# Performance work log

Hardware: AMD Instinct MI355X
Metric: run time of the kernel (lower is better)

## Reference

```python
import jax, jax.numpy as jnp
import numpy as np

N, L, D = 64, 1024, 512
SPAN = 8
LI = L - 2            # inner length after stripping CLS and last token
S = LI // SPAN        # 127 spans per sample
OUT = 300
EPS = 1e-5


def setup_inputs() -> dict:
    key = jax.random.key(0)
    k1, k2, k3 = jax.random.split(key, 3)
    t1 = jax.random.normal(k1, (N, L, D), dtype=jnp.float32)
    # contiguous non-empty spans (start, end) into the inner sequence, same for each sample
    starts = np.arange(S, dtype=np.int64) * SPAN
    ends = starts + SPAN
    word_seq = jnp.asarray(np.broadcast_to(np.stack([starts, ends], -1), (N, S, 2)).copy())
    key_padding_mask = jnp.zeros((N, S), dtype=bool)
    w_lin = jax.random.normal(k2, (OUT, D), dtype=jnp.float32) * (1.0 / np.sqrt(D))
    b_lin = jax.random.normal(k3, (OUT,), dtype=jnp.float32) * 0.02
    gamma = jnp.ones((OUT,), dtype=jnp.float32)
    beta = jnp.zeros((OUT,), dtype=jnp.float32)
    return {"t1": t1, "word_seq": word_seq, "key_padding_mask": key_padding_mask,
            "w_lin": w_lin, "b_lin": b_lin, "gamma": gamma, "beta": beta}


def reference(t1, word_seq, key_padding_mask, w_lin, b_lin, gamma, beta):
    use = t1[:, 0]                      # (N, D) cls token
    inner = t1[:, 1:-1, :]              # (N, LI, D)
    li = inner.shape[1]
    # prefix sums -> span sums via one gather (replaces per-span mean kernels)
    prefix = jnp.concatenate([jnp.zeros_like(inner[:, :1]), jnp.cumsum(inner, axis=1)], axis=1)  # (N, LI+1, D)
    start = jnp.minimum(word_seq[..., 0], li - 1)   # (N, S)
    end = jnp.minimum(word_seq[..., 1], li)
    span_sum = (jnp.take_along_axis(prefix, end[..., None], axis=1)
                - jnp.take_along_axis(prefix, start[..., None], axis=1))  # (N, S, D)
    count = (end - start).astype(inner.dtype)[..., None]                   # (N, S, 1) all > 0
    means = span_sum / count
    # linear_ then LayerNorm
    h = jnp.einsum('nsd,od->nso', means, w_lin) + b_lin                    # (N, S, OUT)
    mu = jnp.mean(h, axis=-1, keepdims=True)
    var = jnp.mean(jnp.square(h - mu), axis=-1, keepdims=True)
    out = (h - mu) * jax.lax.rsqrt(var + EPS) * gamma + beta
    return (out, use)
```

## Files before the change

kernel.cpp:

```cpp
#include <hip/hip_runtime.h>
#include <hip/hip_bf16.h>
#include <stdint.h>

#define N_   64
#define L_   1024
#define D_   512
#define S_   127
#define OUT_ 300
#define NT_  20
#define OUTP (NT_*16)
#define EPS_ 1e-5f
#define M_TOTAL (N_*S_)
#define BM 16
#define BK 64
#define NBLK (M_TOTAL/BM)
#define ASTR 72
#define BSTR 72
#define HSTR 320

typedef __attribute__((ext_vector_type(4))) float  float4v;
typedef __attribute__((ext_vector_type(8))) __bf16 bf16x8;
typedef __attribute__((ext_vector_type(4))) __bf16 bf16x4;

__global__ void conv_w_kernel(const float* __restrict__ w, __bf16* __restrict__ wbf) {
    int idx = blockIdx.x * 256 + threadIdx.x;
    int o = idx >> 9, d = idx & (D_ - 1);
    float v = (o < OUT_) ? w[o * D_ + d] : 0.0f;
    wbf[idx] = (__bf16)v;
}

__global__ void use_copy_kernel(const float* __restrict__ t1, float* __restrict__ ou) {
    int idx = blockIdx.x * 256 + threadIdx.x;
    int n = idx >> 7, dg = idx & 127;
    float4v v = *(const float4v*)(t1 + (size_t)n * L_ * D_ + dg * 4);
    *(float4v*)(ou + n * D_ + dg * 4) = v;
}

__global__ __launch_bounds__(256) void enc_main(
    const float* __restrict__ t1, const int* __restrict__ wseq,
    const __bf16* __restrict__ wbf, const float* __restrict__ b_lin,
    const float* __restrict__ gamma, const float* __restrict__ beta,
    float* __restrict__ out)
{
    __shared__ __align__(16) char smem[BM*ASTR*2 + OUTP*BSTR*2];
    __bf16* Alds = (__bf16*)smem;
    __bf16* Blds = (__bf16*)(smem + BM*ASTR*2);
    float*  hlds = (float*)smem;

    const int tid  = threadIdx.x;
    const int blk  = blockIdx.x;
    const int lane = tid & 63;
    const int wave = tid >> 6;
    const int quad = lane >> 4;
    const int ln16 = lane & 15;

    const int ar  = tid >> 4;
    const int akg = tid & 15;
    const int mg  = blk * BM + ar;
    const int nn  = mg / S_;
    const int st  = min(wseq[mg * 2 + 0], L_ - 3);
    const int en  = min(wseq[mg * 2 + 1], L_ - 2);
    const int cnt = en - st;
    const float inv_cnt = 1.0f / (float)cnt;
    const float* abase = t1 + ((size_t)nn * L_ + 1 + st) * D_ + akg * 4;

    float4v acc[5];
    #pragma unroll
    for (int i = 0; i < 5; ++i) acc[i] = float4v{0.f, 0.f, 0.f, 0.f};

    const int t0 = wave * 5;

    for (int kt = 0; kt < D_ / BK; ++kt) {
        const int k0 = kt * BK;

        float4v s4 = {0.f, 0.f, 0.f, 0.f};
        if (cnt == 8) {
            #pragma unroll
            for (int j = 0; j < 8; ++j)
                s4 += *(const float4v*)(abase + k0 + j * D_);
        } else {
            for (int j = 0; j < cnt; ++j)
                s4 += *(const float4v*)(abase + k0 + j * D_);
        }
        s4 *= inv_cnt;
        bf16x4 a4;
        a4[0] = (__bf16)s4[0]; a4[1] = (__bf16)s4[1];
        a4[2] = (__bf16)s4[2]; a4[3] = (__bf16)s4[3];
        *(bf16x4*)(Alds + ar * ASTR + akg * 4) = a4;

        #pragma unroll
        for (int it = 0; it < 10; ++it) {
            int idx = tid + it * 256;
            int row = idx >> 3, kg = idx & 7;
            bf16x8 v = *(const bf16x8*)(wbf + row * D_ + k0 + kg * 8);
            *(bf16x8*)(Blds + row * BSTR + kg * 8) = v;
        }
        __syncthreads();

        #pragma unroll
        for (int ks = 0; ks < 2; ++ks) {
            const int kk = ks * 32;
            bf16x8 af = *(const bf16x8*)(Alds + ln16 * ASTR + kk + quad * 8);
            #pragma unroll
            for (int i = 0; i < 5; ++i) {
                const int orow = (t0 + i) * 16 + ln16;
                bf16x8 bfr = *(const bf16x8*)(Blds + orow * BSTR + kk + quad * 8);
                acc[i] = __builtin_amdgcn_mfma_f32_16x16x32_bf16(af, bfr, acc[i], 0, 0, 0);
            }
        }
        __syncthreads();
    }

    #pragma unroll
    for (int i = 0; i < 5; ++i) {
        const int col = (t0 + i) * 16 + ln16;
        const float bl = (col < OUT_) ? b_lin[col] : 0.0f;
        #pragma unroll
        for (int r = 0; r < 4; ++r)
            hlds[(quad * 4 + r) * HSTR + col] = acc[i][r] + bl;
    }
    __syncthreads();

    const int r  = tid >> 4;
    const int c0 = tid & 15;
    float sum = 0.f, sq = 0.f;
    #pragma unroll
    for (int i = 0; i < 19; ++i) {
        int c = c0 + 16 * i;
        if (c < OUT_) { float v = hlds[r * HSTR + c]; sum += v; sq += v * v; }
    }
    #pragma unroll
    for (int off = 8; off > 0; off >>= 1) {
        sum += __shfl_xor(sum, off);
        sq  += __shfl_xor(sq,  off);
    }
    const float mu  = sum * (1.0f / OUT_);
    const float var = sq * (1.0f / OUT_) - mu * mu;
    const float rs  = rsqrtf(var + EPS_);
    float* orow = out + (size_t)(blk * BM + r) * OUT_;
    #pragma unroll
    for (int i = 0; i < 19; ++i) {
        int c = c0 + 16 * i;
        if (c < OUT_) {
            float v = hlds[r * HSTR + c];
            orow[c] = (v - mu) * rs * gamma[c] + beta[c];
        }
    }
}

extern "C" void kernel_launch(void* const* d_in, const int* in_sizes, int n_in,
                              void* d_out, int out_size, void* d_ws, size_t ws_size,
                              hipStream_t stream) {
    const float* t1    = (const float*)d_in[0];
    const int*   wseq  = (const int*)d_in[1];
    const float* w_lin = (const float*)d_in[3];
    const float* b_lin = (const float*)d_in[4];
    const float* gamma = (const float*)d_in[5];
    const float* beta  = (const float*)d_in[6];
    float* out  = (float*)d_out;
    __bf16* wbf = (__bf16*)d_ws;

    conv_w_kernel<<<(OUTP * D_) / 256, 256, 0, stream>>>(w_lin, wbf);
    enc_main<<<NBLK, 256, 0, stream>>>(t1, wseq, wbf, b_lin, gamma, beta, out);
    use_copy_kernel<<<(N_ * D_ / 4) / 256, 256, 0, stream>>>(t1, out + (size_t)M_TOTAL * OUT_);
}
```

Before: 211.3 us.

## Split span-mean computation into a separate kernel before the GEMM

Moves the span-mean reduction out of the fused GEMM+LayerNorm kernel into a standalone, fully parallel kernel that writes bf16 means to workspace. The GEMM kernel then loads precomputed A tiles instead of summing eight fp32 rows on every K step. The aim is better memory parallelism for the bandwidth-heavy read of t1, which was serialized with MFMA work inside each block. The cost is an extra launch plus a write and re-read of an intermediate bf16 means buffer of roughly 8 MB.

```diff
diff --git a/kernel.cpp b/kernel.cpp
--- a/kernel.cpp
+++ b/kernel.cpp
@@ -36,11 +36,36 @@
     *(float4v*)(ou + n * D_ + dg * 4) = v;
 }
 
-__global__ __launch_bounds__(256) void enc_main(
+__global__ __launch_bounds__(256) void means_kernel(
     const float* __restrict__ t1, const int* __restrict__ wseq,
-    const __bf16* __restrict__ wbf, const float* __restrict__ b_lin,
-    const float* __restrict__ gamma, const float* __restrict__ beta,
-    float* __restrict__ out)
+    __bf16* __restrict__ means)
+{
+    int idx = blockIdx.x * 256 + threadIdx.x;
+    int m  = idx >> 7;
+    int dg = idx & 127;
+    int st = min(wseq[m * 2 + 0], L_ - 3);
+    int en = min(wseq[m * 2 + 1], L_ - 2);
+    int cnt = en - st;
+    int n = m / S_;
+    const float* base = t1 + ((size_t)n * L_ + 1 + st) * D_ + dg * 4;
+    float4v s = {0.f, 0.f, 0.f, 0.f};
+    if (cnt == 8) {
+        #pragma unroll
+        for (int j = 0; j < 8; ++j) s += *(const float4v*)(base + j * D_);
+    } else {
+        for (int j = 0; j < cnt; ++j) s += *(const float4v*)(base + j * D_);
+    }
+    s *= (1.0f / (float)cnt);
+    bf16x4 a4;
+    a4[0] = (__bf16)s[0]; a4[1] = (__bf16)s[1];
+    a4[2] = (__bf16)s[2]; a4[3] = (__bf16)s[3];
+    *(bf16x4*)(means + (size_t)m * D_ + dg * 4) = a4;
+}
+
+__global__ __launch_bounds__(256) void enc_gemm(
+    const __bf16* __restrict__ means, const __bf16* __restrict__ wbf,
+    const float* __restrict__ b_lin, const float* __restrict__ gamma,
+    const float* __restrict__ beta, float* __restrict__ out)
 {
     __shared__ __align__(16) char smem[BM*ASTR*2 + OUTP*BSTR*2];
     __bf16* Alds = (__bf16*)smem;
@@ -54,16 +79,6 @@
     const int quad = lane >> 4;
     const int ln16 = lane & 15;
 
-    const int ar  = tid >> 4;
-    const int akg = tid & 15;
-    const int mg  = blk * BM + ar;
-    const int nn  = mg / S_;
-    const int st  = min(wseq[mg * 2 + 0], L_ - 3);
-    const int en  = min(wseq[mg * 2 + 1], L_ - 2);
-    const int cnt = en - st;
-    const float inv_cnt = 1.0f / (float)cnt;
-    const float* abase = t1 + ((size_t)nn * L_ + 1 + st) * D_ + akg * 4;
-
     float4v acc[5];
     #pragma unroll
     for (int i = 0; i < 5; ++i) acc[i] = float4v{0.f, 0.f, 0.f, 0.f};
@@ -73,20 +88,11 @@
     for (int kt = 0; kt < D_ / BK; ++kt) {
         const int k0 = kt * BK;
 
-        float4v s4 = {0.f, 0.f, 0.f, 0.f};
-        if (cnt == 8) {
-            #pragma unroll
-            for (int j = 0; j < 8; ++j)
-                s4 += *(const float4v*)(abase + k0 + j * D_);
-        } else {
-            for (int j = 0; j < cnt; ++j)
-                s4 += *(const float4v*)(abase + k0 + j * D_);
+        if (tid < 128) {
+            int row = tid >> 3, kg = tid & 7;
+            bf16x8 v = *(const bf16x8*)(means + (size_t)(blk * BM + row) * D_ + k0 + kg * 8);
+            *(bf16x8*)(Alds + row * ASTR + kg * 8) = v;
         }
-        s4 *= inv_cnt;
-        bf16x4 a4;
-        a4[0] = (__bf16)s4[0]; a4[1] = (__bf16)s4[1];
-        a4[2] = (__bf16)s4[2]; a4[3] = (__bf16)s4[3];
-        *(bf16x4*)(Alds + ar * ASTR + akg * 4) = a4;
 
         #pragma unroll
         for (int it = 0; it < 10; ++it) {
@@ -158,9 +164,11 @@
     const float* gamma = (const float*)d_in[5];
     const float* beta  = (const float*)d_in[6];
     float* out  = (float*)d_out;
-    __bf16* wbf = (__bf16*)d_ws;
+    __bf16* wbf   = (__bf16*)d_ws;
+    __bf16* means = (__bf16*)((char*)d_ws + OUTP * D_ * 2);
 
     conv_w_kernel<<<(OUTP * D_) / 256, 256, 0, stream>>>(w_lin, wbf);
-    enc_main<<<NBLK, 256, 0, stream>>>(t1, wseq, wbf, b_lin, gamma, beta, out);
+    means_kernel<<<(M_TOTAL * (D_ / 4)) / 256, 256, 0, stream>>>(t1, wseq, means);
+    enc_gemm<<<NBLK, 256, 0, stream>>>(means, wbf, b_lin, gamma, beta, out);
     use_copy_kernel<<<(N_ * D_ / 4) / 256, 256, 0, stream>>>(t1, out + (size_t)M_TOTAL * OUT_);
 }
```

After: 220.2 us. 4.2% more time.

## Use single-wave blocks with pre-packed MFMA weight fragments and no LDS

Applied to the files above, without the earlier changes.

The weight conversion kernel now writes bf16 weights already arranged in MFMA fragment order. The main kernel becomes one 64-thread wave per 16-row tile, which computes all 20 output tiles in registers. Each lane reads its A and B fragments straight from global memory, removing the LDS staging, the barriers and the LDS round trip before LayerNorm. The cost is that every block rereads the whole packed weight matrix from cache with no LDS reuse, and register pressure rises with 20 accumulators.

```diff
diff --git a/kernel.cpp b/kernel.cpp
--- a/kernel.cpp
+++ b/kernel.cpp
@@ -11,22 +11,31 @@
 #define OUTP (NT_*16)
 #define EPS_ 1e-5f
 #define M_TOTAL (N_*S_)
-#define BM 16
-#define BK 64
-#define NBLK (M_TOTAL/BM)
-#define ASTR 72
-#define BSTR 72
-#define HSTR 320
+#define NBLK (M_TOTAL/16)
 
 typedef __attribute__((ext_vector_type(4))) float  float4v;
 typedef __attribute__((ext_vector_type(8))) __bf16 bf16x8;
-typedef __attribute__((ext_vector_type(4))) __bf16 bf16x4;
 
-__global__ void conv_w_kernel(const float* __restrict__ w, __bf16* __restrict__ wbf) {
+__global__ void conv_w_pack(const float* __restrict__ w, __bf16* __restrict__ wpk) {
     int idx = blockIdx.x * 256 + threadIdx.x;
-    int o = idx >> 9, d = idx & (D_ - 1);
-    float v = (o < OUT_) ? w[o * D_ + d] : 0.0f;
-    wbf[idx] = (__bf16)v;
+    int t    = idx >> 10;
+    int kt   = (idx >> 7) & 7;
+    int ks   = (idx >> 6) & 1;
+    int quad = (idx >> 4) & 3;
+    int l16  = idx & 15;
+    int o  = t * 16 + l16;
+    int k0 = kt * 64 + ks * 32 + quad * 8;
+    bf16x8 v;
+    if (o < OUT_) {
+        float4v f0 = *(const float4v*)(w + o * D_ + k0);
+        float4v f1 = *(const float4v*)(w + o * D_ + k0 + 4);
+        v[0]=(__bf16)f0[0]; v[1]=(__bf16)f0[1]; v[2]=(__bf16)f0[2]; v[3]=(__bf16)f0[3];
+        v[4]=(__bf16)f1[0]; v[5]=(__bf16)f1[1]; v[6]=(__bf16)f1[2]; v[7]=(__bf16)f1[3];
+    } else {
+        #pragma unroll
+        for (int j = 0; j < 8; ++j) v[j] = (__bf16)0.0f;
+    }
+    *(bf16x8*)(wpk + (size_t)idx * 8) = v;
 }
 
 __global__ void use_copy_kernel(const float* __restrict__ t1, float* __restrict__ ou) {
@@ -36,114 +45,103 @@
     *(float4v*)(ou + n * D_ + dg * 4) = v;
 }
 
-__global__ __launch_bounds__(256) void enc_main(
+__global__ __launch_bounds__(64) void enc_fused(
     const float* __restrict__ t1, const int* __restrict__ wseq,
-    const __bf16* __restrict__ wbf, const float* __restrict__ b_lin,
+    const __bf16* __restrict__ wpk, const float* __restrict__ b_lin,
     const float* __restrict__ gamma, const float* __restrict__ beta,
     float* __restrict__ out)
 {
-    __shared__ __align__(16) char smem[BM*ASTR*2 + OUTP*BSTR*2];
-    __bf16* Alds = (__bf16*)smem;
-    __bf16* Blds = (__bf16*)(smem + BM*ASTR*2);
-    float*  hlds = (float*)smem;
+    const int lane = threadIdx.x;
+    const int ln16 = lane & 15;
+    const int quad = lane >> 4;
+    const int m0   = blockIdx.x * 16;
+    const int m    = m0 + ln16;
 
-    const int tid  = threadIdx.x;
-    const int blk  = blockIdx.x;
-    const int lane = tid & 63;
-    const int wave = tid >> 6;
-    const int quad = lane >> 4;
-    const int ln16 = lane & 15;
-
-    const int ar  = tid >> 4;
-    const int akg = tid & 15;
-    const int mg  = blk * BM + ar;
-    const int nn  = mg / S_;
-    const int st  = min(wseq[mg * 2 + 0], L_ - 3);
-    const int en  = min(wseq[mg * 2 + 1], L_ - 2);
+    const int st  = min(wseq[2 * m],     L_ - 3);
+    const int en  = min(wseq[2 * m + 1], L_ - 2);
     const int cnt = en - st;
     const float inv_cnt = 1.0f / (float)cnt;
-    const float* abase = t1 + ((size_t)nn * L_ + 1 + st) * D_ + akg * 4;
+    const int nn = m / S_;
+    const float* abase = t1 + ((size_t)nn * L_ + 1 + st) * D_ + quad * 8;
 
-    float4v acc[5];
+    float4v acc[NT_];
     #pragma unroll
-    for (int i = 0; i < 5; ++i) acc[i] = float4v{0.f, 0.f, 0.f, 0.f};
+    for (int t = 0; t < NT_; ++t) acc[t] = float4v{0.f, 0.f, 0.f, 0.f};
 
-    const int t0 = wave * 5;
-
-    for (int kt = 0; kt < D_ / BK; ++kt) {
-        const int k0 = kt * BK;
-
-        float4v s4 = {0.f, 0.f, 0.f, 0.f};
+    for (int kt = 0; kt < 8; ++kt) {
+        const int k0 = kt * 64;
+        float4v s0a{0.f,0.f,0.f,0.f}, s0b{0.f,0.f,0.f,0.f};
+        float4v s1a{0.f,0.f,0.f,0.f}, s1b{0.f,0.f,0.f,0.f};
         if (cnt == 8) {
             #pragma unroll
-            for (int j = 0; j < 8; ++j)
-                s4 += *(const float4v*)(abase + k0 + j * D_);
+            for (int j = 0; j < 8; ++j) {
+                const float* p = abase + j * D_ + k0;
+                s0a += *(const float4v*)(p);
+                s0b += *(const float4v*)(p + 4);
+                s1a += *(const float4v*)(p + 32);
+                s1b += *(const float4v*)(p + 36);
+            }
         } else {
-            for (int j = 0; j < cnt; ++j)
-                s4 += *(const float4v*)(abase + k0 + j * D_);
-        }
-        s4 *= inv_cnt;
-        bf16x4 a4;
-        a4[0] = (__bf16)s4[0]; a4[1] = (__bf16)s4[1];
-        a4[2] = (__bf16)s4[2]; a4[3] = (__bf16)s4[3];
-        *(bf16x4*)(Alds + ar * ASTR + akg * 4) = a4;
-
-        #pragma unroll
-        for (int it = 0; it < 10; ++it) {
-            int idx = tid + it * 256;
-            int row = idx >> 3, kg = idx & 7;
-            bf16x8 v = *(const bf16x8*)(wbf + row * D_ + k0 + kg * 8);
-            *(bf16x8*)(Blds + row * BSTR + kg * 8) = v;
-        }
-        __syncthreads();
-
-        #pragma unroll
-        for (int ks = 0; ks < 2; ++ks) {
-            const int kk = ks * 32;
-            bf16x8 af = *(const bf16x8*)(Alds + ln16 * ASTR + kk + quad * 8);
-            #pragma unroll
-            for (int i = 0; i < 5; ++i) {
-                const int orow = (t0 + i) * 16 + ln16;
-                bf16x8 bfr = *(const bf16x8*)(Blds + orow * BSTR + kk + quad * 8);
-                acc[i] = __builtin_amdgcn_mfma_f32_16x16x32_bf16(af, bfr, acc[i], 0, 0, 0);
+            for (int j = 0; j < cnt; ++j) {
+                const float* p = abase + j * D_ + k0;
+                s0a += *(const float4v*)(p);
+                s0b += *(const float4v*)(p + 4);
+                s1a += *(const float4v*)(p + 32);
+                s1b += *(const float4v*)(p + 36);
             }
         }
-        __syncthreads();
+        s0a *= inv_cnt; s0b *= inv_cnt; s1a *= inv_cnt; s1b *= inv_cnt;
+        bf16x8 af0, af1;
+        af0[0]=(__bf16)s0a[0]; af0[1]=(__bf16)s0a[1]; af0[2]=(__bf16)s0a[2]; af0[3]=(__bf16)s0a[3];
+        af0[4]=(__bf16)s0b[0]; af0[5]=(__bf16)s0b[1]; af0[6]=(__bf16)s0b[2]; af0[7]=(__bf16)s0b[3];
+        af1[0]=(__bf16)s1a[0]; af1[1]=(__bf16)s1a[1]; af1[2]=(__bf16)s1a[2]; af1[3]=(__bf16)s1a[3];
+        af1[4]=(__bf16)s1b[0]; af1[5]=(__bf16)s1b[1]; af1[6]=(__bf16)s1b[2]; af1[7]=(__bf16)s1b[3];
+
+        const __bf16* bp = wpk + ((size_t)kt * 128 + lane) * 8;
+        #pragma unroll
+        for (int t = 0; t < NT_; ++t) {
+            bf16x8 b0 = *(const bf16x8*)(bp + t * 8192);
+            acc[t] = __builtin_amdgcn_mfma_f32_16x16x32_bf16(af0, b0, acc[t], 0, 0, 0);
+            bf16x8 b1 = *(const bf16x8*)(bp + t * 8192 + 512);
+            acc[t] = __builtin_amdgcn_mfma_f32_16x16x32_bf16(af1, b1, acc[t], 0, 0, 0);
+        }
     }
 
+    float bl[NT_];
     #pragma unroll
-    for (int i = 0; i < 5; ++i) {
-        const int col = (t0 + i) * 16 + ln16;
-        const float bl = (col < OUT_) ? b_lin[col] : 0.0f;
+    for (int t = 0; t < NT_; ++t) {
+        int col = t * 16 + ln16;
+        bl[t] = (col < OUT_) ? b_lin[col] : 0.0f;
+    }
+    float mu[4], rs[4];
+    #pragma unroll
+    for (int r = 0; r < 4; ++r) {
+        float sum = 0.f, sq = 0.f;
         #pragma unroll
-        for (int r = 0; r < 4; ++r)
-            hlds[(quad * 4 + r) * HSTR + col] = acc[i][r] + bl;
-    }
-    __syncthreads();
-
-    const int r  = tid >> 4;
-    const int c0 = tid & 15;
-    float sum = 0.f, sq = 0.f;
-    #pragma unroll
-    for (int i = 0; i < 19; ++i) {
-        int c = c0 + 16 * i;
-        if (c < OUT_) { float v = hlds[r * HSTR + c]; sum += v; sq += v * v; }
+        for (int t = 0; t < NT_; ++t) {
+            float h = acc[t][r] + bl[t];
+            sum += h; sq += h * h;
+        }
+        #pragma unroll
+        for (int off = 8; off > 0; off >>= 1) {
+            sum += __shfl_xor(sum, off);
+            sq  += __shfl_xor(sq,  off);
+        }
+        mu[r] = sum * (1.0f / OUT_);
+        float var = sq * (1.0f / OUT_) - mu[r] * mu[r];
+        rs[r] = rsqrtf(var + EPS_);
     }
     #pragma unroll
-    for (int off = 8; off > 0; off >>= 1) {
-        sum += __shfl_xor(sum, off);
-        sq  += __shfl_xor(sq,  off);
-    }
-    const float mu  = sum * (1.0f / OUT_);
-    const float var = sq * (1.0f / OUT_) - mu * mu;
-    const float rs  = rsqrtf(var + EPS_);
-    float* orow = out + (size_t)(blk * BM + r) * OUT_;
-    #pragma unroll
-    for (int i = 0; i < 19; ++i) {
-        int c = c0 + 16 * i;
-        if (c < OUT_) {
-            float v = hlds[r * HSTR + c];
-            orow[c] = (v - mu) * rs * gamma[c] + beta[c];
+    for (int t = 0; t < 19; ++t) {
+        int col = t * 16 + ln16;
+        if (col < OUT_) {
+            float g = gamma[col], be = beta[col];
+            #pragma unroll
+            for (int r = 0; r < 4; ++r) {
+                int gm = m0 + quad * 4 + r;
+                float h = acc[t][r] + bl[t];
+                out[(size_t)gm * OUT_ + col] = (h - mu[r]) * rs[r] * g + be;
+            }
         }
     }
 }
@@ -158,9 +156,9 @@
     const float* gamma = (const float*)d_in[5];
     const float* beta  = (const float*)d_in[6];
     float* out  = (float*)d_out;
-    __bf16* wbf = (__bf16*)d_ws;
+    __bf16* wpk = (__bf16*)d_ws;
 
-    conv_w_kernel<<<(OUTP * D_) / 256, 256, 0, stream>>>(w_lin, wbf);
-    enc_main<<<NBLK, 256, 0, stream>>>(t1, wseq, wbf, b_lin, gamma, beta, out);
+    conv_w_pack<<<(NT_ * 1024) / 256, 256, 0, stream>>>(w_lin, wpk);
+    enc_fused<<<NBLK, 64, 0, stream>>>(t1, wseq, wpk, b_lin, gamma, beta, out);
     use_copy_kernel<<<(N_ * D_ / 4) / 256, 256, 0, stream>>>(t1, out + (size_t)M_TOTAL * OUT_);
 }
```

Measured after the change: 220.8 us. +4.5%, slower.

## Prepack weights in MFMA fragment order and read B directly from global

Applied to the files above, without the earlier changes.

The weight conversion now writes bf16 weights in the exact per-lane MFMA fragment layout, so the main kernel loads B operands straight from global/L2 instead of staging them through LDS. All span means for a 16-row tile are computed up front into LDS with one barrier, which removes the per-K-step syncthreads pairs. The CLS copy is merged into the prep kernel, so there is one fewer launch. The cost is that every block re-reads the packed weights from global memory, and the new LDS layout is padded.

```diff
diff --git a/kernel.cpp b/kernel.cpp
--- a/kernel.cpp
+++ b/kernel.cpp
@@ -11,40 +11,54 @@
 #define OUTP (NT_*16)
 #define EPS_ 1e-5f
 #define M_TOTAL (N_*S_)
-#define BM 16
-#define BK 64
-#define NBLK (M_TOTAL/BM)
-#define ASTR 72
-#define BSTR 72
-#define HSTR 320
+#define NBLK (M_TOTAL/16)
+#define AST  520
+#define HSTR 325
+#define PACK_BLOCKS 80
+#define COPY_BLOCKS 32
 
 typedef __attribute__((ext_vector_type(4))) float  float4v;
 typedef __attribute__((ext_vector_type(8))) __bf16 bf16x8;
 typedef __attribute__((ext_vector_type(4))) __bf16 bf16x4;
 
-__global__ void conv_w_kernel(const float* __restrict__ w, __bf16* __restrict__ wbf) {
-    int idx = blockIdx.x * 256 + threadIdx.x;
-    int o = idx >> 9, d = idx & (D_ - 1);
-    float v = (o < OUT_) ? w[o * D_ + d] : 0.0f;
-    wbf[idx] = (__bf16)v;
+__global__ void prep_kernel(const float* __restrict__ w, __bf16* __restrict__ wpk,
+                            const float* __restrict__ t1, float* __restrict__ ouse) {
+    if (blockIdx.x < PACK_BLOCKS) {
+        int idx = blockIdx.x * 256 + threadIdx.x;
+        int t    = idx >> 10;
+        int kt   = (idx >> 7) & 7;
+        int ks   = (idx >> 6) & 1;
+        int quad = (idx >> 4) & 3;
+        int l16  = idx & 15;
+        int o  = t * 16 + l16;
+        int k0 = kt * 64 + ks * 32 + quad * 8;
+        bf16x8 v;
+        if (o < OUT_) {
+            float4v f0 = *(const float4v*)(w + o * D_ + k0);
+            float4v f1 = *(const float4v*)(w + o * D_ + k0 + 4);
+            v[0]=(__bf16)f0[0]; v[1]=(__bf16)f0[1]; v[2]=(__bf16)f0[2]; v[3]=(__bf16)f0[3];
+            v[4]=(__bf16)f1[0]; v[5]=(__bf16)f1[1]; v[6]=(__bf16)f1[2]; v[7]=(__bf16)f1[3];
+        } else {
+            #pragma unroll
+            for (int j = 0; j < 8; ++j) v[j] = (__bf16)0.0f;
+        }
+        *(bf16x8*)(wpk + (size_t)idx * 8) = v;
+    } else {
+        int idx = (blockIdx.x - PACK_BLOCKS) * 256 + threadIdx.x;
+        int n = idx >> 7, dg = idx & 127;
+        float4v v = *(const float4v*)(t1 + (size_t)n * L_ * D_ + dg * 4);
+        *(float4v*)(ouse + n * D_ + dg * 4) = v;
+    }
 }
 
-__global__ void use_copy_kernel(const float* __restrict__ t1, float* __restrict__ ou) {
-    int idx = blockIdx.x * 256 + threadIdx.x;
-    int n = idx >> 7, dg = idx & 127;
-    float4v v = *(const float4v*)(t1 + (size_t)n * L_ * D_ + dg * 4);
-    *(float4v*)(ou + n * D_ + dg * 4) = v;
-}
-
-__global__ __launch_bounds__(256) void enc_main(
+__global__ __launch_bounds__(256) void enc_fused(
     const float* __restrict__ t1, const int* __restrict__ wseq,
-    const __bf16* __restrict__ wbf, const float* __restrict__ b_lin,
+    const __bf16* __restrict__ wpk, const float* __restrict__ b_lin,
     const float* __restrict__ gamma, const float* __restrict__ beta,
     float* __restrict__ out)
 {
-    __shared__ __align__(16) char smem[BM*ASTR*2 + OUTP*BSTR*2];
+    __shared__ __align__(16) char smem[16 * HSTR * 4];
     __bf16* Alds = (__bf16*)smem;
-    __bf16* Blds = (__bf16*)(smem + BM*ASTR*2);
     float*  hlds = (float*)smem;
 
     const int tid  = threadIdx.x;
@@ -54,62 +68,54 @@
     const int quad = lane >> 4;
     const int ln16 = lane & 15;
 
-    const int ar  = tid >> 4;
-    const int akg = tid & 15;
-    const int mg  = blk * BM + ar;
-    const int nn  = mg / S_;
-    const int st  = min(wseq[mg * 2 + 0], L_ - 3);
-    const int en  = min(wseq[mg * 2 + 1], L_ - 2);
-    const int cnt = en - st;
-    const float inv_cnt = 1.0f / (float)cnt;
-    const float* abase = t1 + ((size_t)nn * L_ + 1 + st) * D_ + akg * 4;
+    {
+        const int row = tid >> 4;
+        const int kg  = tid & 15;
+        const int m   = blk * 16 + row;
+        const int st  = min(wseq[2 * m],     L_ - 3);
+        const int en  = min(wseq[2 * m + 1], L_ - 2);
+        const int cnt = en - st;
+        const float inv_cnt = 1.0f / (float)cnt;
+        const int nn = m / S_;
+        const float* base = t1 + ((size_t)nn * L_ + 1 + st) * D_ + kg * 4;
+        #pragma unroll
+        for (int c = 0; c < 8; ++c) {
+            const int k0 = c * 64;
+            float4v s = {0.f, 0.f, 0.f, 0.f};
+            if (cnt == 8) {
+                #pragma unroll
+                for (int j = 0; j < 8; ++j) s += *(const float4v*)(base + j * D_ + k0);
+            } else {
+                for (int j = 0; j < cnt; ++j) s += *(const float4v*)(base + j * D_ + k0);
+            }
+            s *= inv_cnt;
+            bf16x4 a4;
+            a4[0]=(__bf16)s[0]; a4[1]=(__bf16)s[1]; a4[2]=(__bf16)s[2]; a4[3]=(__bf16)s[3];
+            *(bf16x4*)(Alds + row * AST + k0 + kg * 4) = a4;
+        }
+    }
+    __syncthreads();
 
     float4v acc[5];
     #pragma unroll
     for (int i = 0; i < 5; ++i) acc[i] = float4v{0.f, 0.f, 0.f, 0.f};
-
     const int t0 = wave * 5;
 
-    for (int kt = 0; kt < D_ / BK; ++kt) {
-        const int k0 = kt * BK;
-
-        float4v s4 = {0.f, 0.f, 0.f, 0.f};
-        if (cnt == 8) {
-            #pragma unroll
-            for (int j = 0; j < 8; ++j)
-                s4 += *(const float4v*)(abase + k0 + j * D_);
-        } else {
-            for (int j = 0; j < cnt; ++j)
-                s4 += *(const float4v*)(abase + k0 + j * D_);
+    #pragma unroll 2
+    for (int kt = 0; kt < 8; ++kt) {
+        bf16x8 af0 = *(const bf16x8*)(Alds + ln16 * AST + kt * 64 + quad * 8);
+        bf16x8 af1 = *(const bf16x8*)(Alds + ln16 * AST + kt * 64 + 32 + quad * 8);
+        const __bf16* bp = wpk + ((size_t)kt * 128 + lane) * 8;
+        #pragma unroll
+        for (int i = 0; i < 5; ++i) {
+            const __bf16* bt = bp + (size_t)(t0 + i) * 8192;
+            bf16x8 b0 = *(const bf16x8*)(bt);
+            acc[i] = __builtin_amdgcn_mfma_f32_16x16x32_bf16(af0, b0, acc[i], 0, 0, 0);
+            bf16x8 b1 = *(const bf16x8*)(bt + 512);
+            acc[i] = __builtin_amdgcn_mfma_f32_16x16x32_bf16(af1, b1, acc[i], 0, 0, 0);
         }
-        s4 *= inv_cnt;
-        bf16x4 a4;
-        a4[0] = (__bf16)s4[0]; a4[1] = (__bf16)s4[1];
-        a4[2] = (__bf16)s4[2]; a4[3] = (__bf16)s4[3];
-        *(bf16x4*)(Alds + ar * ASTR + akg * 4) = a4;
-
-        #pragma unroll
-        for (int it = 0; it < 10; ++it) {
-            int idx = tid + it * 256;
-            int row = idx >> 3, kg = idx & 7;
-            bf16x8 v = *(const bf16x8*)(wbf + row * D_ + k0 + kg * 8);
-            *(bf16x8*)(Blds + row * BSTR + kg * 8) = v;
-        }
-        __syncthreads();
-
-        #pragma unroll
-        for (int ks = 0; ks < 2; ++ks) {
-            const int kk = ks * 32;
-            bf16x8 af = *(const bf16x8*)(Alds + ln16 * ASTR + kk + quad * 8);
-            #pragma unroll
-            for (int i = 0; i < 5; ++i) {
-                const int orow = (t0 + i) * 16 + ln16;
-                bf16x8 bfr = *(const bf16x8*)(Blds + orow * BSTR + kk + quad * 8);
-                acc[i] = __builtin_amdgcn_mfma_f32_16x16x32_bf16(af, bfr, acc[i], 0, 0, 0);
-            }
-        }
-        __syncthreads();
     }
+    __syncthreads();
 
     #pragma unroll
     for (int i = 0; i < 5; ++i) {
@@ -137,7 +143,7 @@
     const float mu  = sum * (1.0f / OUT_);
     const float var = sq * (1.0f / OUT_) - mu * mu;
     const float rs  = rsqrtf(var + EPS_);
-    float* orow = out + (size_t)(blk * BM + r) * OUT_;
+    float* orow = out + (size_t)(blk * 16 + r) * OUT_;
     #pragma unroll
     for (int i = 0; i < 19; ++i) {
         int c = c0 + 16 * i;
@@ -158,9 +164,9 @@
     const float* gamma = (const float*)d_in[5];
     const float* beta  = (const float*)d_in[6];
     float* out  = (float*)d_out;
-    __bf16* wbf = (__bf16*)d_ws;
+    __bf16* wpk = (__bf16*)d_ws;
 
-    conv_w_kernel<<<(OUTP * D_) / 256, 256, 0, stream>>>(w_lin, wbf);
-    enc_main<<<NBLK, 256, 0, stream>>>(t1, wseq, wbf, b_lin, gamma, beta, out);
-    use_copy_kernel<<<(N_ * D_ / 4) / 256, 256, 0, stream>>>(t1, out + (size_t)M_TOTAL * OUT_);
+    prep_kernel<<<PACK_BLOCKS + COPY_BLOCKS, 256, 0, stream>>>(
+        w_lin, wpk, t1, out + (size_t)M_TOTAL * OUT_);
+    enc_fused<<<NBLK, 256, 0, stream>>>(t1, wseq, wpk, b_lin, gamma, beta, out);
 }
```

After: 213.3 us. No clear change (+0.9%).
